# Kernel optimization log

Measured on AMD Instinct MI355X. Metric: run time of the kernel, lower is better.

## Reference

```python
import jax, jax.numpy as jnp
import numpy as np

B, NC, CH, HF, WF = 2, 6, 256, 32, 88
N, CIN = 100000, 128
VOXEL_SIZE = jnp.array([0.075, 0.075, 0.2], dtype=jnp.float32)
PC_MIN = jnp.array([-54.0, -54.0, -5.0], dtype=jnp.float32)
DOWNSAMPLE = 8.0
DMIN, DMAX = 1.0, 60.0


def setup_inputs() -> dict:
    key = jax.random.key(0)
    ks = jax.random.split(key, 12)
    # voxel coords: (batch, z, y, x), batch column sorted to match the
    # original per-batch-loop concatenation order
    b = jnp.repeat(jnp.arange(B, dtype=jnp.int32), N // B)
    x = jax.random.randint(ks[0], (N,), 0, 1440, dtype=jnp.int32)
    y = jax.random.randint(ks[1], (N,), 0, 1440, dtype=jnp.int32)
    z = jax.random.randint(ks[2], (N,), 0, 40, dtype=jnp.int32)
    voxel_coords = jnp.stack([b, z, y, x], axis=1)
    voxel_features = jax.random.normal(ks[3], (N, CIN), dtype=jnp.float32)
    img_feats = jax.random.normal(ks[4], (B, NC, CH, HF, WF), dtype=jnp.float32)
    # pinhole intrinsics for a 704x256 image
    K = jnp.array([[500.0, 0.0, 352.0], [0.0, 500.0, 128.0], [0.0, 0.0, 1.0]], dtype=jnp.float32)
    intrins = K + 0.01 * jax.random.normal(ks[5], (B, NC, 3, 3), dtype=jnp.float32)
    post_rots = 0.5 * jnp.eye(3, dtype=jnp.float32) + 0.001 * jax.random.normal(ks[6], (B, NC, 3, 3), dtype=jnp.float32)
    post_trans = 0.01 * jax.random.normal(ks[7], (B, NC, 3), dtype=jnp.float32)
    # bda: near-identity 4x4
    bda = jnp.tile(jnp.eye(4, dtype=jnp.float32), (B, 1, 1))
    bda = bda.at[:, :3, :3].add(0.01 * jax.random.normal(ks[8], (B, 3, 3), dtype=jnp.float32))
    bda = bda.at[:, :3, 3].set(0.1 * jax.random.normal(ks[9], (B, 3), dtype=jnp.float32))
    # lidar->cam: standard axis permutation (x->z) so depth is positive for half the scene
    R = jnp.array([[0.0, -1.0, 0.0], [0.0, 0.0, -1.0], [1.0, 0.0, 0.0]], dtype=jnp.float32)
    l2c = jnp.tile(jnp.eye(4, dtype=jnp.float32), (B, NC, 1, 1))
    l2c = l2c.at[..., :3, :3].set(R + 0.01 * jax.random.normal(ks[10], (B, NC, 3, 3), dtype=jnp.float32))
    l2c = l2c.at[..., :3, 3].set(0.1 * jax.random.normal(ks[11], (B, NC, 3), dtype=jnp.float32))
    W = 0.02 * jax.random.normal(jax.random.fold_in(key, 99), (CIN, CH), dtype=jnp.float32)
    return dict(voxel_features=voxel_features, voxel_coords=voxel_coords, img_feats=img_feats,
                intrins=intrins, post_rots=post_rots, post_trans=post_trans, bda=bda,
                lidar2cam=l2c, W=W)


def reference(voxel_features, voxel_coords, img_feats, intrins, post_rots, post_trans, bda, lidar2cam, W):
    bidx = voxel_coords[:, 0]
    # voxel index (x,y,z) -> metric lidar coords
    p = voxel_coords[:, jnp.array([3, 2, 1])].astype(jnp.float32) * VOXEL_SIZE + PC_MIN  # [N,3]
    # undo bda augmentation: (p - t) @ inv(R).T
    binv = jnp.linalg.inv(bda[:, :3, :3])  # [B,3,3]
    pcam = jnp.einsum('nj,nij->ni', p - bda[bidx, :3, 3], binv[bidx])  # [N,3]
    # lidar2img = cam2img @ lidar2cam.T (faithful to original, incl. full 4x4 transpose)
    cam2img = jnp.tile(jnp.eye(4, dtype=intrins.dtype), (B, NC, 1, 1)).at[..., :3, :3].set(intrins)
    L = cam2img @ jnp.swapaxes(lidar2cam, -1, -2)  # [B,NC,4,4]
    Lv = L[bidx]  # [N,NC,4,4]
    pimg = jnp.einsum('nj,ncij->nci', pcam, Lv[:, :, :3, :3]) + Lv[:, :, :3, 3]  # [N,NC,3]
    pimg = jnp.concatenate([pimg[..., :2] / pimg[..., 2:3], pimg[..., 2:3]], axis=-1)
    pimg = jnp.einsum('ncj,ncij->nci', pimg, post_rots[bidx]) + post_trans[bidx]
    # gather_img_feature: round/clip + masked gather, scatter into zeros == multiply by mask
    coor = jnp.round(pimg[..., :2] / DOWNSAMPLE)
    depth = pimg[..., 2]
    mask = ((coor[..., 0] >= 0) & (coor[..., 0] < WF) & (coor[..., 1] >= 0) & (coor[..., 1] < HF)
            & (depth < DMAX) & (depth >= DMIN))  # [N,NC]
    xi = jnp.clip(coor[..., 0].astype(jnp.int32), 0, WF - 1)
    yi = jnp.clip(coor[..., 1].astype(jnp.int32), 0, HF - 1)
    cams = jnp.arange(NC)[None, :]
    g = img_feats[bidx[:, None], cams, :, yi, xi]  # [N,NC,CH]
    g = g * mask[..., None].astype(g.dtype)
    # sum over cameras, then Linear(256 -> CIN, no bias)
    img_voxel = jnp.einsum('nc,oc->no', g.sum(axis=1), W)  # [N,CIN]
    out_feats = jnp.concatenate([voxel_features, img_voxel], axis=0)  # [2N,CIN]
    out_coords = jnp.concatenate([voxel_coords, voxel_coords], axis=0)  # [2N,4]
    return out_feats, out_coords
```

## Files before the change

### kernel.cpp

```cpp
#include <hip/hip_runtime.h>
#include <math.h>

#define BB   2
#define NCAM 6
#define CH   256
#define HF   32
#define WF   88
#define NV   100000
#define CIN  128
#define VPB  32

typedef __attribute__((ext_vector_type(8))) short short8;
typedef __attribute__((ext_vector_type(4))) float f32x4;

static __device__ inline short f2bf(float f) {
    union { float f; unsigned u; } v; v.f = f;
    unsigned r = (v.u + 0x7fffu + ((v.u >> 16) & 1u)) >> 16;
    return (short)r;
}
static __device__ inline float bflo(unsigned int pk) {
    union { unsigned int u; float f; } a; a.u = pk << 16; return a.f;
}
static __device__ inline float bfhi(unsigned int pk) {
    union { unsigned int u; float f; } a; a.u = pk & 0xffff0000u; return a.f;
}

__global__ void prep_params_w(const float* __restrict__ intrins,
                              const float* __restrict__ post_rots,
                              const float* __restrict__ post_trans,
                              const float* __restrict__ bda,
                              const float* __restrict__ l2c,
                              const float* __restrict__ W,
                              double* __restrict__ params,
                              short*  __restrict__ Wbf)
{
    if (blockIdx.x > 0) {
        int chunk = blockIdx.x - 1;
        int l = threadIdx.x;
        int nt = chunk >> 3, kk = chunk & 7;
        int n = nt * 16 + (l & 15);
        int k = kk * 32 + (l >> 4) * 8;
        short v[8];
        #pragma unroll
        for (int j = 0; j < 8; j++) v[j] = f2bf(W[n * CH + k + j]);
        *(short8*)(Wbf + ((size_t)chunk * 64 + l) * 8) = *(short8*)v;
        return;
    }

    int t = threadIdx.x;
    if (t >= BB * NCAM) return;
    int b = t / NCAM;

    const float* Bm = bda + b * 16;
    double a00 = Bm[0], a01 = Bm[1], a02 = Bm[2],  tx = Bm[3];
    double a10 = Bm[4], a11 = Bm[5], a12 = Bm[6],  ty = Bm[7];
    double a20 = Bm[8], a21 = Bm[9], a22 = Bm[10], tz = Bm[11];

    double det = a00*(a11*a22 - a12*a21) - a01*(a10*a22 - a12*a20) + a02*(a10*a21 - a11*a20);
    double id  = 1.0 / det;
    double inv[3][3];
    inv[0][0] =  (a11*a22 - a12*a21) * id;
    inv[0][1] = -(a01*a22 - a02*a21) * id;
    inv[0][2] =  (a01*a12 - a02*a11) * id;
    inv[1][0] = -(a10*a22 - a12*a20) * id;
    inv[1][1] =  (a00*a22 - a02*a20) * id;
    inv[1][2] = -(a00*a12 - a02*a10) * id;
    inv[2][0] =  (a10*a21 - a11*a20) * id;
    inv[2][1] = -(a00*a21 - a01*a20) * id;
    inv[2][2] =  (a00*a11 - a01*a10) * id;

    const float* In = intrins + t * 9;
    const float* Lc = l2c + t * 16;

    double M3[3][3];
    #pragma unroll
    for (int i = 0; i < 3; i++)
        #pragma unroll
        for (int j = 0; j < 3; j++)
            M3[i][j] = (double)In[i*3+0] * (double)Lc[j*4+0]
                     + (double)In[i*3+1] * (double)Lc[j*4+1]
                     + (double)In[i*3+2] * (double)Lc[j*4+2];

    double M[3][3];
    #pragma unroll
    for (int i = 0; i < 3; i++)
        #pragma unroll
        for (int j = 0; j < 3; j++)
            M[i][j] = M3[i][0]*inv[0][j] + M3[i][1]*inv[1][j] + M3[i][2]*inv[2][j];

    double* P = params + t * 24;
    #pragma unroll
    for (int i = 0; i < 3; i++)
        #pragma unroll
        for (int j = 0; j < 3; j++)
            P[i*3+j] = M[i][j];
    #pragma unroll
    for (int i = 0; i < 3; i++)
        P[9+i] = -(M[i][0]*tx + M[i][1]*ty + M[i][2]*tz);
    #pragma unroll
    for (int i = 0; i < 9; i++) P[12+i] = (double)post_rots[t*9 + i];
    #pragma unroll
    for (int i = 0; i < 3; i++) P[21+i] = (double)post_trans[t*3 + i];
}

__global__ __launch_bounds__(256) void transpose_img(const float* __restrict__ img,
                                                     unsigned short* __restrict__ imgT)
{
    __shared__ float tile[32][89];
    int bid = blockIdx.x;
    int cg  = bid & 7;
    int y   = (bid >> 3) & 31;
    int bc  = bid >> 8;
    int t   = threadIdx.x;

    const float* src = img + ((size_t)(bc * CH + cg * 32)) * (HF * WF) + y * WF;
    #pragma unroll
    for (int i = 0; i < 11; i++) {
        int lin = i * 256 + t;
        int ch  = lin / 88;
        int x   = lin - ch * 88;
        tile[ch][x] = src[(size_t)ch * (HF * WF) + x];
    }
    __syncthreads();

    unsigned short* dst = imgT + ((size_t)(bc * HF + y) * WF) * CH + cg * 32;
    #pragma unroll
    for (int j = 0; j < 6; j++) {
        int lin2 = j * 256 + t;
        if (j == 5 && t >= 128) break;
        int x  = lin2 >> 4;
        int cp = lin2 & 15;
        unsigned short lo = (unsigned short)f2bf(tile[2 * cp][x]);
        unsigned short hi = (unsigned short)f2bf(tile[2 * cp + 1][x]);
        unsigned int pk = (unsigned int)lo | ((unsigned int)hi << 16);
        *(unsigned int*)(dst + (size_t)x * CH + 2 * cp) = pk;
    }
}

struct POF { int o; float m; };

template <bool TRANS>
__global__ __launch_bounds__(256) void fused_gather_mm(
    const float*  __restrict__ vf,
    const int*    __restrict__ coords,
    const void*   __restrict__ imgv,
    const double* __restrict__ params,
    const short*  __restrict__ Wbf,
    float*        __restrict__ out)
{
    const int t  = threadIdx.x;
    const int n0 = blockIdx.x * VPB;

    {
        const float4* vf4 = (const float4*)vf;
        float4*       o4  = (float4*)out;
        int base = n0 * (CIN / 4);
        #pragma unroll
        for (int i = 0; i < 4; i++)
            o4[base + i * 256 + t] = vf4[base + i * 256 + t];
    }
    if (t < VPB * 4) {
        int gi = n0 * 4 + t;
        float cv = (float)coords[gi];
        const size_t cb = (size_t)2 * NV * CIN;
        out[cb + gi]                  = cv;
        out[cb + (size_t)NV * 4 + gi] = cv;
    }

    __shared__ POF pof[VPB][NCAM];
    __shared__ __align__(16) short aFrag[16 * 64 * 8];

    if (t < VPB * NCAM) {
        int vi = t / NCAM, c = t - vi * NCAM;
        int n  = n0 + vi;
        int b  = coords[n * 4 + 0];
        int zi = coords[n * 4 + 1];
        int yi = coords[n * 4 + 2];
        int xi = coords[n * 4 + 3];
        double px = (double)xi * (double)0.075f + (-54.0);
        double py = (double)yi * (double)0.075f + (-54.0);
        double pz = (double)zi * (double)0.2f   + (-5.0);
        const double* P = params + (b * NCAM + c) * 24;
        double X = P[0]*px + P[1]*py + P[2]*pz + P[9];
        double Y = P[3]*px + P[4]*py + P[5]*pz + P[10];
        double Z = P[6]*px + P[7]*py + P[8]*pz + P[11];
        double u = X / Z;
        double v = Y / Z;
        double q0 = P[12]*u + P[13]*v + P[14]*Z + P[21];
        double q1 = P[15]*u + P[16]*v + P[17]*Z + P[22];
        double q2 = P[18]*u + P[19]*v + P[20]*Z + P[23];
        double cx = rint(q0 * 0.125);
        double cy = rint(q1 * 0.125);
        bool m = (cx >= 0.0) && (cx < (double)WF) && (cy >= 0.0) && (cy < (double)HF)
              && (q2 < 60.0) && (q2 >= 1.0);
        int o = 0;
        if (m) {
            int ix = (int)cx, iy = (int)cy;
            if (TRANS) o = ((b * NCAM + c) * HF + iy) * WF + ix;
            else       o = (b * NCAM + c) * (CH * HF * WF) + iy * WF + ix;
        }
        POF p2; p2.o = o; p2.m = m ? 1.0f : 0.0f;
        pof[vi][c] = p2;
    }
    __syncthreads();

    {
        const int l   = t & 63;
        const int w   = t >> 6;
        const int vt  = w >> 1;
        const int kb  = (w & 1) * 4;
        const int vi  = vt * 16 + (l & 15);
        const int q   = l >> 4;

        float g[4][8];
        #pragma unroll
        for (int i = 0; i < 4; i++)
            #pragma unroll
            for (int j = 0; j < 8; j++) g[i][j] = 0.0f;

        if (TRANS) {
            const unsigned short* imgT = (const unsigned short*)imgv;
            #pragma unroll
            for (int c = 0; c < NCAM; c++) {
                POF p2 = pof[vi][c];
                float wm = p2.m;
                const unsigned short* px = imgT + (size_t)p2.o * CH + q * 8;
                #pragma unroll
                for (int k2 = 0; k2 < 4; k2++) {
                    uint4 A = *(const uint4*)(px + (kb + k2) * 32);
                    g[k2][0] = fmaf(wm, bflo(A.x), g[k2][0]);
                    g[k2][1] = fmaf(wm, bfhi(A.x), g[k2][1]);
                    g[k2][2] = fmaf(wm, bflo(A.y), g[k2][2]);
                    g[k2][3] = fmaf(wm, bfhi(A.y), g[k2][3]);
                    g[k2][4] = fmaf(wm, bflo(A.z), g[k2][4]);
                    g[k2][5] = fmaf(wm, bfhi(A.z), g[k2][5]);
                    g[k2][6] = fmaf(wm, bflo(A.w), g[k2][6]);
                    g[k2][7] = fmaf(wm, bfhi(A.w), g[k2][7]);
                }
            }
        } else {
            const float* img = (const float*)imgv;
            #pragma unroll
            for (int c = 0; c < NCAM; c++) {
                POF p2 = pof[vi][c];
                float wm = p2.m;
                #pragma unroll
                for (int k2 = 0; k2 < 4; k2++) {
                    int k0 = (kb + k2) * 32 + q * 8;
                    #pragma unroll
                    for (int j = 0; j < 8; j++)
                        g[k2][j] = fmaf(wm, img[(size_t)(k0 + j) * (HF * WF) + p2.o], g[k2][j]);
                }
            }
        }

        #pragma unroll
        for (int k2 = 0; k2 < 4; k2++) {
            short tmp[8];
            #pragma unroll
            for (int j = 0; j < 8; j++) tmp[j] = f2bf(g[k2][j]);
            int chunk = vt * 8 + kb + k2;
            *(short8*)(aFrag + (chunk * 64 + l) * 8) = *(short8*)tmp;
        }
    }
    __syncthreads();

    {
        const int w    = t >> 6;
        const int lane = t & 63;
        f32x4 acc[2][2];
        #pragma unroll
        for (int a2 = 0; a2 < 2; a2++)
            #pragma unroll
            for (int b2 = 0; b2 < 2; b2++)
                acc[a2][b2] = (f32x4){0.f, 0.f, 0.f, 0.f};
        const short8* Bf = (const short8*)Wbf;
        #pragma unroll
        for (int kk = 0; kk < 8; kk++) {
            short8 b0 = Bf[((2 * w)     * 8 + kk) * 64 + lane];
            short8 b1 = Bf[((2 * w + 1) * 8 + kk) * 64 + lane];
            short8 a0 = *(const short8*)(aFrag + ((0 * 8 + kk) * 64 + lane) * 8);
            short8 a1 = *(const short8*)(aFrag + ((1 * 8 + kk) * 64 + lane) * 8);
            acc[0][0] = __builtin_amdgcn_mfma_f32_16x16x32_bf16(a0, b0, acc[0][0], 0, 0, 0);
            acc[0][1] = __builtin_amdgcn_mfma_f32_16x16x32_bf16(a0, b1, acc[0][1], 0, 0, 0);
            acc[1][0] = __builtin_amdgcn_mfma_f32_16x16x32_bf16(a1, b0, acc[1][0], 0, 0, 0);
            acc[1][1] = __builtin_amdgcn_mfma_f32_16x16x32_bf16(a1, b1, acc[1][1], 0, 0, 0);
        }
        float* oiv = out + (size_t)NV * CIN;
        int col = lane & 15, rq = lane >> 4;
        #pragma unroll
        for (int a2 = 0; a2 < 2; a2++) {
            #pragma unroll
            for (int r = 0; r < 4; r++) {
                int n = n0 + a2 * 16 + rq * 4 + r;
                oiv[(size_t)n * CIN + (2 * w)     * 16 + col] = acc[a2][0][r];
                oiv[(size_t)n * CIN + (2 * w + 1) * 16 + col] = acc[a2][1][r];
            }
        }
    }
}

extern "C" void kernel_launch(void* const* d_in, const int* in_sizes, int n_in,
                              void* d_out, int out_size, void* d_ws, size_t ws_size,
                              hipStream_t stream)
{
    const float* vf      = (const float*)d_in[0];
    const int*   coords  = (const int*)d_in[1];
    const float* img     = (const float*)d_in[2];
    const float* intrins = (const float*)d_in[3];
    const float* prots   = (const float*)d_in[4];
    const float* ptrans  = (const float*)d_in[5];
    const float* bda     = (const float*)d_in[6];
    const float* l2c     = (const float*)d_in[7];
    const float* W       = (const float*)d_in[8];
    float* out = (float*)d_out;

    double* params = (double*)d_ws;
    const size_t wbf_off  = 4096;
    const size_t wbf_sz   = (size_t)8 * 8 * 64 * 8 * sizeof(short);
    const size_t imgT_off = wbf_off + wbf_sz;
    const size_t needed   = imgT_off + (size_t)BB * NCAM * HF * WF * CH * sizeof(unsigned short);

    short* Wbf = (short*)((char*)d_ws + wbf_off);

    prep_params_w<<<65, 64, 0, stream>>>(intrins, prots, ptrans, bda, l2c, W, params, Wbf);

    if (ws_size >= needed) {
        unsigned short* imgT = (unsigned short*)((char*)d_ws + imgT_off);
        transpose_img<<<BB * NCAM * HF * 8, 256, 0, stream>>>(img, imgT);
        fused_gather_mm<true><<<NV / VPB, 256, 0, stream>>>(vf, coords, imgT, params, Wbf, out);
    } else {
        fused_gather_mm<false><<<NV / VPB, 256, 0, stream>>>(vf, coords, img, params, Wbf, out);
    }
}
```

Before: 219.1 us.

## Project image pixels through the linear layer before gathering per voxel

Uses linearity to apply the 256->128 weight matrix once per image pixel (33792 pixels) with MFMA, storing a bf16 projected image. The per-voxel kernel then only gathers and sums 128-channel projected rows over cameras, skipping masked cameras. This removes the per-voxel matmul and halves the gathered bytes, and it replaces the transpose kernel. The cost is rounding the projected result to bf16 instead of the summed features, and the per-voxel fallback path when workspace is small is dropped. VPB is also raised to 40 voxels per block.

Result: faster. 210.7 us, median of 2 (-3.9%).

```diff
diff --git a/kernel.cpp b/kernel.cpp
--- a/kernel.cpp
+++ b/kernel.cpp
@@ -4,11 +4,13 @@
 #define BB   2
 #define NCAM 6
 #define CH   256
+#define COUT 128
 #define HF   32
 #define WF   88
+#define NPIX (BB * NCAM * HF * WF)
 #define NV   100000
 #define CIN  128
-#define VPB  32
+#define VPB  40
 
 typedef __attribute__((ext_vector_type(8))) short short8;
 typedef __attribute__((ext_vector_type(4))) float f32x4;
@@ -103,50 +105,53 @@
     for (int i = 0; i < 3; i++) P[21+i] = (double)post_trans[t*3 + i];
 }
 
-__global__ __launch_bounds__(256) void transpose_img(const float* __restrict__ img,
-                                                     unsigned short* __restrict__ imgT)
-{
-    __shared__ float tile[32][89];
-    int bid = blockIdx.x;
-    int cg  = bid & 7;
-    int y   = (bid >> 3) & 31;
-    int bc  = bid >> 8;
-    int t   = threadIdx.x;
-
-    const float* src = img + ((size_t)(bc * CH + cg * 32)) * (HF * WF) + y * WF;
-    #pragma unroll
-    for (int i = 0; i < 11; i++) {
-        int lin = i * 256 + t;
-        int ch  = lin / 88;
-        int x   = lin - ch * 88;
-        tile[ch][x] = src[(size_t)ch * (HF * WF) + x];
-    }
-    __syncthreads();
-
-    unsigned short* dst = imgT + ((size_t)(bc * HF + y) * WF) * CH + cg * 32;
-    #pragma unroll
-    for (int j = 0; j < 6; j++) {
-        int lin2 = j * 256 + t;
-        if (j == 5 && t >= 128) break;
-        int x  = lin2 >> 4;
-        int cp = lin2 & 15;
-        unsigned short lo = (unsigned short)f2bf(tile[2 * cp][x]);
-        unsigned short hi = (unsigned short)f2bf(tile[2 * cp + 1][x]);
-        unsigned int pk = (unsigned int)lo | ((unsigned int)hi << 16);
-        *(unsigned int*)(dst + (size_t)x * CH + 2 * cp) = pk;
-    }
+__global__ __launch_bounds__(256) void pixel_mm(const float* __restrict__ img,
+                                                const short* __restrict__ Wbf,
+                                                unsigned short* __restrict__ imgP)
+{
+    const int w    = (blockIdx.x << 2) + (threadIdx.x >> 6);
+    const int lane = threadIdx.x & 63;
+    const int bc   = w / 176;
+    const int pt   = w - bc * 176;
+    const int pix0 = pt * 16;
+
+    const float* A0 = img + (size_t)bc * (CH * HF * WF) + pix0 + (lane & 15);
+    const int q8 = (lane >> 4) * 8;
+
+    f32x4 acc[8];
+    #pragma unroll
+    for (int nt = 0; nt < 8; nt++) acc[nt] = (f32x4){0.f, 0.f, 0.f, 0.f};
+
+    const short8* Bf = (const short8*)Wbf;
+    for (int kk = 0; kk < 8; kk++) {
+        short av[8];
+        #pragma unroll
+        for (int j = 0; j < 8; j++)
+            av[j] = f2bf(A0[(size_t)(kk * 32 + q8 + j) * (HF * WF)]);
+        short8 a = *(short8*)av;
+        #pragma unroll
+        for (int nt = 0; nt < 8; nt++)
+            acc[nt] = __builtin_amdgcn_mfma_f32_16x16x32_bf16(
+                          a, Bf[(nt * 8 + kk) * 64 + lane], acc[nt], 0, 0, 0);
+    }
+
+    const int col = lane & 15, rq = lane >> 4;
+    unsigned short* P0 = imgP + ((size_t)bc * (HF * WF) + pix0 + rq * 4) * COUT + col;
+    #pragma unroll
+    for (int nt = 0; nt < 8; nt++)
+        #pragma unroll
+        for (int r = 0; r < 4; r++)
+            P0[(size_t)r * COUT + nt * 16] = (unsigned short)f2bf(acc[nt][r]);
 }
 
 struct POF { int o; float m; };
 
-template <bool TRANS>
-__global__ __launch_bounds__(256) void fused_gather_mm(
-    const float*  __restrict__ vf,
-    const int*    __restrict__ coords,
-    const void*   __restrict__ imgv,
-    const double* __restrict__ params,
-    const short*  __restrict__ Wbf,
-    float*        __restrict__ out)
+__global__ __launch_bounds__(256) void voxel_gather(
+    const float*          __restrict__ vf,
+    const int*            __restrict__ coords,
+    const unsigned short* __restrict__ imgP,
+    const double*         __restrict__ params,
+    float*                __restrict__ out)
 {
     const int t  = threadIdx.x;
     const int n0 = blockIdx.x * VPB;
@@ -156,7 +161,7 @@
         float4*       o4  = (float4*)out;
         int base = n0 * (CIN / 4);
         #pragma unroll
-        for (int i = 0; i < 4; i++)
+        for (int i = 0; i < 5; i++)
             o4[base + i * 256 + t] = vf4[base + i * 256 + t];
     }
     if (t < VPB * 4) {
@@ -168,7 +173,6 @@
     }
 
     __shared__ POF pof[VPB][NCAM];
-    __shared__ __align__(16) short aFrag[16 * 64 * 8];
 
     if (t < VPB * NCAM) {
         int vi = t / NCAM, c = t - vi * NCAM;
@@ -196,107 +200,30 @@
         int o = 0;
         if (m) {
             int ix = (int)cx, iy = (int)cy;
-            if (TRANS) o = ((b * NCAM + c) * HF + iy) * WF + ix;
-            else       o = (b * NCAM + c) * (CH * HF * WF) + iy * WF + ix;
+            o = ((b * NCAM + c) * HF + iy) * WF + ix;
         }
         POF p2; p2.o = o; p2.m = m ? 1.0f : 0.0f;
         pof[vi][c] = p2;
     }
     __syncthreads();
 
-    {
-        const int l   = t & 63;
-        const int w   = t >> 6;
-        const int vt  = w >> 1;
-        const int kb  = (w & 1) * 4;
-        const int vi  = vt * 16 + (l & 15);
-        const int q   = l >> 4;
-
-        float g[4][8];
-        #pragma unroll
-        for (int i = 0; i < 4; i++)
-            #pragma unroll
-            for (int j = 0; j < 8; j++) g[i][j] = 0.0f;
-
-        if (TRANS) {
-            const unsigned short* imgT = (const unsigned short*)imgv;
-            #pragma unroll
-            for (int c = 0; c < NCAM; c++) {
-                POF p2 = pof[vi][c];
-                float wm = p2.m;
-                const unsigned short* px = imgT + (size_t)p2.o * CH + q * 8;
-                #pragma unroll
-                for (int k2 = 0; k2 < 4; k2++) {
-                    uint4 A = *(const uint4*)(px + (kb + k2) * 32);
-                    g[k2][0] = fmaf(wm, bflo(A.x), g[k2][0]);
-                    g[k2][1] = fmaf(wm, bfhi(A.x), g[k2][1]);
-                    g[k2][2] = fmaf(wm, bflo(A.y), g[k2][2]);
-                    g[k2][3] = fmaf(wm, bfhi(A.y), g[k2][3]);
-                    g[k2][4] = fmaf(wm, bflo(A.z), g[k2][4]);
-                    g[k2][5] = fmaf(wm, bfhi(A.z), g[k2][5]);
-                    g[k2][6] = fmaf(wm, bflo(A.w), g[k2][6]);
-                    g[k2][7] = fmaf(wm, bfhi(A.w), g[k2][7]);
-                }
-            }
-        } else {
-            const float* img = (const float*)imgv;
-            #pragma unroll
-            for (int c = 0; c < NCAM; c++) {
-                POF p2 = pof[vi][c];
-                float wm = p2.m;
-                #pragma unroll
-                for (int k2 = 0; k2 < 4; k2++) {
-                    int k0 = (kb + k2) * 32 + q * 8;
-                    #pragma unroll
-                    for (int j = 0; j < 8; j++)
-                        g[k2][j] = fmaf(wm, img[(size_t)(k0 + j) * (HF * WF) + p2.o], g[k2][j]);
-                }
+    const int h = t >> 5, l32 = t & 31;
+    #pragma unroll
+    for (int vv = 0; vv < 5; vv++) {
+        int vi = h * 5 + vv;
+        float a0 = 0.f, a1 = 0.f, a2 = 0.f, a3 = 0.f;
+        #pragma unroll
+        for (int c = 0; c < NCAM; c++) {
+            POF p2 = pof[vi][c];
+            if (p2.m != 0.0f) {
+                const unsigned short* px = imgP + (size_t)p2.o * COUT + l32 * 4;
+                uint2 A = *(const uint2*)px;
+                a0 += bflo(A.x); a1 += bfhi(A.x);
+                a2 += bflo(A.y); a3 += bfhi(A.y);
             }
         }
-
-        #pragma unroll
-        for (int k2 = 0; k2 < 4; k2++) {
-            short tmp[8];
-            #pragma unroll
-            for (int j = 0; j < 8; j++) tmp[j] = f2bf(g[k2][j]);
-            int chunk = vt * 8 + kb + k2;
-            *(short8*)(aFrag + (chunk * 64 + l) * 8) = *(short8*)tmp;
-        }
-    }
-    __syncthreads();
-
-    {
-        const int w    = t >> 6;
-        const int lane = t & 63;
-        f32x4 acc[2][2];
-        #pragma unroll
-        for (int a2 = 0; a2 < 2; a2++)
-            #pragma unroll
-            for (int b2 = 0; b2 < 2; b2++)
-                acc[a2][b2] = (f32x4){0.f, 0.f, 0.f, 0.f};
-        const short8* Bf = (const short8*)Wbf;
-        #pragma unroll
-        for (int kk = 0; kk < 8; kk++) {
-            short8 b0 = Bf[((2 * w)     * 8 + kk) * 64 + lane];
-            short8 b1 = Bf[((2 * w + 1) * 8 + kk) * 64 + lane];
-            short8 a0 = *(const short8*)(aFrag + ((0 * 8 + kk) * 64 + lane) * 8);
-            short8 a1 = *(const short8*)(aFrag + ((1 * 8 + kk) * 64 + lane) * 8);
-            acc[0][0] = __builtin_amdgcn_mfma_f32_16x16x32_bf16(a0, b0, acc[0][0], 0, 0, 0);
-            acc[0][1] = __builtin_amdgcn_mfma_f32_16x16x32_bf16(a0, b1, acc[0][1], 0, 0, 0);
-            acc[1][0] = __builtin_amdgcn_mfma_f32_16x16x32_bf16(a1, b0, acc[1][0], 0, 0, 0);
-            acc[1][1] = __builtin_amdgcn_mfma_f32_16x16x32_bf16(a1, b1, acc[1][1], 0, 0, 0);
-        }
-        float* oiv = out + (size_t)NV * CIN;
-        int col = lane & 15, rq = lane >> 4;
-        #pragma unroll
-        for (int a2 = 0; a2 < 2; a2++) {
-            #pragma unroll
-            for (int r = 0; r < 4; r++) {
-                int n = n0 + a2 * 16 + rq * 4 + r;
-                oiv[(size_t)n * CIN + (2 * w)     * 16 + col] = acc[a2][0][r];
-                oiv[(size_t)n * CIN + (2 * w + 1) * 16 + col] = acc[a2][1][r];
-            }
-        }
+        float4 r4 = {a0, a1, a2, a3};
+        *(float4*)(out + ((size_t)NV + n0 + vi) * CIN + l32 * 4) = r4;
     }
 }
 
@@ -318,18 +245,12 @@
     double* params = (double*)d_ws;
     const size_t wbf_off  = 4096;
     const size_t wbf_sz   = (size_t)8 * 8 * 64 * 8 * sizeof(short);
-    const size_t imgT_off = wbf_off + wbf_sz;
-    const size_t needed   = imgT_off + (size_t)BB * NCAM * HF * WF * CH * sizeof(unsigned short);
-
-    short* Wbf = (short*)((char*)d_ws + wbf_off);
+    const size_t imgP_off = wbf_off + wbf_sz;
+
+    short*          Wbf  = (short*)((char*)d_ws + wbf_off);
+    unsigned short* imgP = (unsigned short*)((char*)d_ws + imgP_off);
 
     prep_params_w<<<65, 64, 0, stream>>>(intrins, prots, ptrans, bda, l2c, W, params, Wbf);
-
-    if (ws_size >= needed) {
-        unsigned short* imgT = (unsigned short*)((char*)d_ws + imgT_off);
-        transpose_img<<<BB * NCAM * HF * 8, 256, 0, stream>>>(img, imgT);
-        fused_gather_mm<true><<<NV / VPB, 256, 0, stream>>>(vf, coords, imgT, params, Wbf, out);
-    } else {
-        fused_gather_mm<false><<<NV / VPB, 256, 0, stream>>>(vf, coords, img, params, Wbf, out);
-    }
-}
+    pixel_mm<<<(12 * 176) / 4, 256, 0, stream>>>(img, Wbf, imgP);
+    voxel_gather<<<NV / VPB, 256, 0, stream>>>(vf, coords, imgP, params, out);
+}
```
